# Kernel optimization log

Hardware: AMD Instinct MI355X
Metric: run time of the kernel (lower is better)

## Reference

```python
import jax, jax.numpy as jnp
import numpy as np

B, F, H, W = 2, 8, 16, 16
S = F * H * W                 # 2048 tokens
DIM, NH = 2048, 16
HD = DIM // NH                # 128
C = HD // 2                   # 64 complex pairs per head
CT = C - 2 * (C // 3)         # 22 temporal freqs
CH = C // 3                   # 21 height / 21 width freqs
L = 1024                      # freq table length
SHIFT = 4                     # TCROPE_SHIFT
EPS = 1e-6


def setup_inputs():
    key = jax.random.key(0)
    ks = jax.random.split(key, 12)
    lin = lambda k: jax.random.normal(k, (DIM, DIM), jnp.float32) / np.sqrt(DIM)
    x = jax.random.normal(ks[0], (B, S, DIM), jnp.float32)
    q_w, k_w, v_w, o_w = lin(ks[1]), lin(ks[2]), lin(ks[3]), lin(ks[4])
    q_b = jax.random.normal(ks[5], (DIM,), jnp.float32) * 0.02
    k_b = jax.random.normal(ks[6], (DIM,), jnp.float32) * 0.02
    v_b = jax.random.normal(ks[7], (DIM,), jnp.float32) * 0.02
    o_b = jax.random.normal(ks[8], (DIM,), jnp.float32) * 0.02
    norm_q_w = jnp.ones((DIM,), jnp.float32)
    norm_k_w = jnp.ones((DIM,), jnp.float32)
    # unit-magnitude complex rotations stored as (cos, sin): [L, C, 2]
    inv = 1.0 / (10000.0 ** (np.arange(C, dtype=np.float32) / C))
    ang = np.arange(L, dtype=np.float32)[:, None] * inv[None, :]
    freqs = jnp.asarray(np.stack([np.cos(ang), np.sin(ang)], axis=-1))
    seq_lens = jnp.full((B,), S, jnp.int32)
    grid_sizes = jnp.tile(jnp.array([[F, H, W]], jnp.int32), (B, 1))
    inner_t = jnp.array([[4, 4], [3, 5]], jnp.int32)  # per-sample shot lengths, sum == F
    return dict(x=x, q_w=q_w, q_b=q_b, k_w=k_w, k_b=k_b, v_w=v_w, v_b=v_b,
                o_w=o_w, o_b=o_b, norm_q_w=norm_q_w, norm_k_w=norm_k_w,
                freqs=freqs, seq_lens=seq_lens, grid_sizes=grid_sizes, inner_t=inner_t)


def _rmsnorm(x, w):
    return x * jax.lax.rsqrt(jnp.mean(x * x, axis=-1, keepdims=True) + EPS) * w


def _rope(x, freqs, inner_t, seq_lens):
    # x: [B,S,NH,HD]; per-sample 3D RoPE over (f,h,w) with per-shot temporal index shift.
    xr = x.reshape(B, S, NH, C, 2)
    f0, f1, f2 = freqs[:, :CT], freqs[:, CT:CT + CH], freqs[:, CT + CH:]
    t = jnp.arange(F)
    # frame t belongs to shot j  =>  temporal freq index = j*SHIFT + t  (matches freq_select)
    shot = jax.vmap(lambda it: jnp.searchsorted(jnp.cumsum(it), t, side='right'))(inner_t)
    t_idx = shot * SHIFT + t[None, :]                                   # [B,F]
    tf = jnp.broadcast_to(f0[t_idx][:, :, None, None], (B, F, H, W, CT, 2))
    hf = jnp.broadcast_to(f1[:H][None, None, :, None], (B, F, H, W, CH, 2))
    wf = jnp.broadcast_to(f2[:W][None, None, None, :], (B, F, H, W, CH, 2))
    fr = jnp.concatenate([tf, hf, wf], axis=-2).reshape(B, S, 1, C, 2)  # [B,S,1,C,2]
    a, b = xr[..., 0], xr[..., 1]
    cr, ci = fr[..., 0], fr[..., 1]
    rot = jnp.stack([a * cr - b * ci, a * ci + b * cr], axis=-1).reshape(B, S, NH, HD)
    # positions past f*h*w are left un-rotated in the original (tail concat)
    keep = (jnp.arange(S)[None, :] < seq_lens[:, None])[:, :, None, None]
    return jnp.where(keep, rot, x)


def reference(x, q_w, q_b, k_w, k_b, v_w, v_b, o_w, o_b,
              norm_q_w, norm_k_w, freqs, seq_lens, grid_sizes, inner_t):
    # grid_sizes is (F,H,W) for every sample; baked in as static constants above.
    q = _rmsnorm(x @ q_w + q_b, norm_q_w).reshape(B, S, NH, HD)
    k = _rmsnorm(x @ k_w + k_b, norm_k_w).reshape(B, S, NH, HD)
    v = (x @ v_w + v_b).reshape(B, S, NH, HD)
    q = _rope(q, freqs, inner_t, seq_lens)
    k = _rope(k, freqs, inner_t, seq_lens)
    scores = jnp.einsum('bqnd,bknd->bnqk', q, k) * (HD ** -0.5)
    kmask = (jnp.arange(S)[None, :] < seq_lens[:, None])[:, None, None, :]
    scores = jnp.where(kmask, scores, -1e30)
    attn = jax.nn.softmax(scores, axis=-1)
    out = jnp.einsum('bnqk,bknd->bqnd', attn, v).reshape(B, S, DIM)
    return out @ o_w + o_b
```

## Files before the change

### kernel.cpp

```cpp
#include <hip/hip_runtime.h>


typedef __attribute__((ext_vector_type(8))) short bf16x8;
typedef __attribute__((ext_vector_type(4))) float f32x4;

__device__ __forceinline__ unsigned short f2bf(float f) {
  unsigned int u = __builtin_bit_cast(unsigned int, f);
  u = (u + 0x7FFFu + ((u >> 16) & 1u)) >> 16;
  return (unsigned short)u;
}
__device__ __forceinline__ float bf2f(unsigned short h) {
  unsigned int u = ((unsigned int)h) << 16;
  return __builtin_bit_cast(float, u);
}

#define GLOAD16(gp, lp)                                                        \
  __builtin_amdgcn_global_load_lds(                                            \
      (__attribute__((address_space(1))) void*)(gp),                           \
      (__attribute__((address_space(3))) void*)(lp), 16, 0, 0)

__global__ __launch_bounds__(256) void k_convert(const float* __restrict__ in,
                                                 unsigned short* __restrict__ out,
                                                 int n8) {
  int i = blockIdx.x * 256 + threadIdx.x;
  const int stride = gridDim.x * 256;
  for (; i < n8; i += stride) {
    const float4* p = (const float4*)in + (size_t)i * 2;
    float4 a = p[0], b = p[1];
    bf16x8 v;
    v[0] = (short)f2bf(a.x); v[1] = (short)f2bf(a.y);
    v[2] = (short)f2bf(a.z); v[3] = (short)f2bf(a.w);
    v[4] = (short)f2bf(b.x); v[5] = (short)f2bf(b.y);
    v[6] = (short)f2bf(b.z); v[7] = (short)f2bf(b.w);
    *(bf16x8*)(out + (size_t)i * 8) = v;
  }
}

__global__ __launch_bounds__(256) void k_transpose(const float* __restrict__ in,
                                                   unsigned short* __restrict__ out,
                                                   int R, int C) {
  __shared__ float tile[32][33];
  const int c0 = blockIdx.x * 32, r0 = blockIdx.y * 32;
  const int tx = threadIdx.x, ty = threadIdx.y;
#pragma unroll
  for (int i = 0; i < 4; i++)
    tile[ty + i * 8][tx] = in[(size_t)(r0 + ty + i * 8) * C + c0 + tx];
  __syncthreads();
#pragma unroll
  for (int i = 0; i < 4; i++)
    out[(size_t)(c0 + ty + i * 8) * R + r0 + tx] = f2bf(tile[tx][ty + i * 8]);
}

template <int OUTF32, int BIASMODE>
__global__ __launch_bounds__(256) void k_gemm(const unsigned short* __restrict__ A,
                                              const unsigned short* __restrict__ BT,
                                              void* __restrict__ Cout,
                                              const float* __restrict__ bias,
                                              int M, int N, int K) {
  __shared__ unsigned short As[128 * 32];
  __shared__ unsigned short Bs[128 * 32];
  const int tid = threadIdx.x;
  const int lane = tid & 63, w = tid >> 6;
  const int g = lane >> 4, cc = lane & 15;
  const int gx = gridDim.x;
  int id = blockIdx.y * gx + blockIdx.x;
  const int tot = gx * gridDim.y;
  id = (id & 7) * (tot >> 3) + (id >> 3);
  const int n0 = (id % gx) * 128, m0 = (id / gx) * 128;
  const int wm = (w >> 1) * 64, wn = (w & 1) * 64;
  f32x4 acc[4][4] = {};
  const unsigned short* Ab = A + (size_t)m0 * K;
  const unsigned short* Bb = BT + (size_t)n0 * K;
  const int r0 = tid >> 2, c0 = (tid & 3) * 8;
  for (int kt = 0; kt < K; kt += 32) {
    GLOAD16(Ab + (size_t)r0 * K + kt + c0, As + tid * 8);
    GLOAD16(Ab + (size_t)(r0 + 64) * K + kt + c0, As + (tid + 256) * 8);
    GLOAD16(Bb + (size_t)r0 * K + kt + c0, Bs + tid * 8);
    GLOAD16(Bb + (size_t)(r0 + 64) * K + kt + c0, Bs + (tid + 256) * 8);
    __syncthreads();
    bf16x8 af[4], bfr[4];
#pragma unroll
    for (int m4 = 0; m4 < 4; m4++)
      af[m4] = *(const bf16x8*)(As + (wm + m4 * 16 + cc) * 32 + g * 8);
#pragma unroll
    for (int n4 = 0; n4 < 4; n4++)
      bfr[n4] = *(const bf16x8*)(Bs + (wn + n4 * 16 + cc) * 32 + g * 8);
#pragma unroll
    for (int m4 = 0; m4 < 4; m4++)
#pragma unroll
      for (int n4 = 0; n4 < 4; n4++)
        acc[m4][n4] = __builtin_amdgcn_mfma_f32_16x16x32_bf16(af[m4], bfr[n4],
                                                              acc[m4][n4], 0, 0, 0);
    __syncthreads();
  }
#pragma unroll
  for (int m4 = 0; m4 < 4; m4++)
#pragma unroll
    for (int n4 = 0; n4 < 4; n4++) {
      const int col = n0 + wn + n4 * 16 + cc;
#pragma unroll
      for (int r = 0; r < 4; r++) {
        const int row = m0 + wm + m4 * 16 + g * 4 + r;
        float v = acc[m4][n4][r];
        if (BIASMODE == 1) v += bias[row];
        if (BIASMODE == 2) v += bias[col];
        if (OUTF32)
          ((float*)Cout)[(size_t)row * N + col] = v;
        else
          ((unsigned short*)Cout)[(size_t)row * N + col] = f2bf(v);
      }
    }
}

__device__ __forceinline__ void stage_half(const unsigned short* __restrict__ src,
                                           int K, unsigned short* dst, int tid) {
#pragma unroll
  for (int j = 0; j < 2; j++) {
    const int li = tid + j * 512;
    const int r = li >> 3;
    const int c16 = (li & 7) ^ (r & 7);
    GLOAD16(src + (size_t)r * K + c16 * 8, (char*)dst + li * 16);
  }
}

__global__ __launch_bounds__(512, 2) void k_gemm_yqk(const unsigned short* __restrict__ A,
                                                     const unsigned short* __restrict__ BT,
                                                     unsigned short* __restrict__ Cout) {
  __shared__ unsigned short As[2][256 * 64];
  __shared__ unsigned short Bs[2][256 * 64];
  const int tid = threadIdx.x;
  const int lane = tid & 63, w = tid >> 6;
  const int g = lane >> 4, cc = lane & 15;
  const int wm = (w >> 2) * 128, wn = (w & 3) * 64;
  const int swz = (cc & 7) << 4;
  const int N = 4096, K = 2048;
  int id = blockIdx.x;
  id = (id & 7) * 32 + (id >> 3);
  const int m0 = (id >> 4) * 256, n0 = (id & 15) * 256;
  f32x4 acc[8][4] = {};
  const int T = K >> 6;

  stage_half(BT + (size_t)n0 * K, K, Bs[0], tid);
  stage_half(A + (size_t)m0 * K, K, As[0], tid);
  stage_half(BT + (size_t)(n0 + 128) * K, K, Bs[0] + 8192, tid);
  stage_half(A + (size_t)(m0 + 128) * K, K, As[0] + 8192, tid);
  stage_half(BT + (size_t)n0 * K + 64, K, Bs[1], tid);
  stage_half(A + (size_t)m0 * K + 64, K, As[1], tid);
  asm volatile("s_waitcnt vmcnt(4)" ::: "memory");
  __builtin_amdgcn_s_barrier();

  for (int t = 0; t < T; ++t) {
    const int c = t & 1;
    const char* Ac = (const char*)As[c];
    const char* Bc = (const char*)Bs[c];
    bf16x8 ar[4][2], br[4][2];
#pragma unroll
    for (int m = 0; m < 4; m++)
#pragma unroll
      for (int kk = 0; kk < 2; kk++)
        ar[m][kk] = *(const bf16x8*)(Ac + (wm + m * 16 + cc) * 128 +
                                     ((kk * 64 + g * 16) ^ swz));
#pragma unroll
    for (int n = 0; n < 2; n++)
#pragma unroll
      for (int kk = 0; kk < 2; kk++)
        br[n][kk] = *(const bf16x8*)(Bc + (wn + n * 16 + cc) * 128 +
                                     ((kk * 64 + g * 16) ^ swz));
    stage_half(BT + (size_t)(n0 + 128) * K + ((t + 1) & (T - 1)) * 64, K,
               Bs[c ^ 1] + 8192, tid);
    __builtin_amdgcn_s_barrier();
    asm volatile("s_waitcnt lgkmcnt(0)" ::: "memory");
    __builtin_amdgcn_sched_barrier(0);
    __builtin_amdgcn_s_setprio(1);
#pragma unroll
    for (int kk = 0; kk < 2; kk++)
#pragma unroll
      for (int m = 0; m < 4; m++)
#pragma unroll
        for (int n = 0; n < 2; n++)
          acc[m][n] = __builtin_amdgcn_mfma_f32_16x16x32_bf16(ar[m][kk], br[n][kk],
                                                              acc[m][n], 0, 0, 0);
    __builtin_amdgcn_s_setprio(0);
    __builtin_amdgcn_s_barrier();
#pragma unroll
    for (int n = 2; n < 4; n++)
#pragma unroll
      for (int kk = 0; kk < 2; kk++)
        br[n][kk] = *(const bf16x8*)(Bc + (wn + n * 16 + cc) * 128 +
                                     ((kk * 64 + g * 16) ^ swz));
    stage_half(A + (size_t)(m0 + 128) * K + ((t + 1) & (T - 1)) * 64, K,
               As[c ^ 1] + 8192, tid);
    __builtin_amdgcn_s_barrier();
    asm volatile("s_waitcnt lgkmcnt(0)" ::: "memory");
    __builtin_amdgcn_sched_barrier(0);
    __builtin_amdgcn_s_setprio(1);
#pragma unroll
    for (int kk = 0; kk < 2; kk++)
#pragma unroll
      for (int m = 0; m < 4; m++)
#pragma unroll
        for (int n = 2; n < 4; n++)
          acc[m][n] = __builtin_amdgcn_mfma_f32_16x16x32_bf16(ar[m][kk], br[n][kk],
                                                              acc[m][n], 0, 0, 0);
    __builtin_amdgcn_s_setprio(0);
    __builtin_amdgcn_s_barrier();
#pragma unroll
    for (int m = 0; m < 4; m++)
#pragma unroll
      for (int kk = 0; kk < 2; kk++)
        ar[m][kk] = *(const bf16x8*)(Ac + (wm + (m + 4) * 16 + cc) * 128 +
                                     ((kk * 64 + g * 16) ^ swz));
    stage_half(BT + (size_t)n0 * K + ((t + 2) & (T - 1)) * 64, K, Bs[c], tid);
    __builtin_amdgcn_s_barrier();
    asm volatile("s_waitcnt lgkmcnt(0)" ::: "memory");
    __builtin_amdgcn_sched_barrier(0);
    __builtin_amdgcn_s_setprio(1);
#pragma unroll
    for (int kk = 0; kk < 2; kk++)
#pragma unroll
      for (int m = 0; m < 4; m++)
#pragma unroll
        for (int n = 0; n < 2; n++)
          acc[m + 4][n] = __builtin_amdgcn_mfma_f32_16x16x32_bf16(ar[m][kk], br[n][kk],
                                                                  acc[m + 4][n], 0, 0, 0);
    __builtin_amdgcn_s_setprio(0);
    __builtin_amdgcn_s_barrier();
    stage_half(A + (size_t)m0 * K + ((t + 2) & (T - 1)) * 64, K, As[c], tid);
    __builtin_amdgcn_s_setprio(1);
#pragma unroll
    for (int kk = 0; kk < 2; kk++)
#pragma unroll
      for (int m = 0; m < 4; m++)
#pragma unroll
        for (int n = 2; n < 4; n++)
          acc[m + 4][n] = __builtin_amdgcn_mfma_f32_16x16x32_bf16(ar[m][kk], br[n][kk],
                                                                  acc[m + 4][n], 0, 0, 0);
    __builtin_amdgcn_s_setprio(0);
    if (t < T - 2)
      asm volatile("s_waitcnt vmcnt(4)" ::: "memory");
    else
      asm volatile("s_waitcnt vmcnt(0)" ::: "memory");
    __builtin_amdgcn_sched_barrier(0);
    __builtin_amdgcn_s_barrier();
  }

#pragma unroll
  for (int mi = 0; mi < 8; mi++)
#pragma unroll
    for (int n = 0; n < 4; n++) {
      const int col = n0 + wn + n * 16 + cc;
#pragma unroll
      for (int j = 0; j < 4; j++) {
        const int row = m0 + wm + mi * 16 + g * 4 + j;
        Cout[(size_t)row * N + col] = f2bf(acc[mi][n][j]);
      }
    }
}

__global__ __launch_bounds__(256) void k_qk_epi(const unsigned short* __restrict__ Yqk,
                                                const float* __restrict__ q_b,
                                                const float* __restrict__ k_b,
                                                const float* __restrict__ nqw,
                                                const float* __restrict__ nkw,
                                                const float* __restrict__ freqs,
                                                const int* __restrict__ inner_t,
                                                unsigned short* __restrict__ Q,
                                                unsigned short* __restrict__ K) {
  const int row = blockIdx.x;
  const int b = row >> 11, s = row & 2047;
  const int t = threadIdx.x;
  const unsigned short* yr = Yqk + (size_t)row * 4096;
  bf16x8 yq = *(const bf16x8*)(yr + t * 8);
  bf16x8 yk = *(const bf16x8*)(yr + 2048 + t * 8);
  float4 qb0 = *(const float4*)(q_b + t * 8), qb1 = *(const float4*)(q_b + t * 8 + 4);
  float4 kb0 = *(const float4*)(k_b + t * 8), kb1 = *(const float4*)(k_b + t * 8 + 4);
  float q[8], k[8];
  q[0] = bf2f((unsigned short)yq[0]) + qb0.x; q[1] = bf2f((unsigned short)yq[1]) + qb0.y;
  q[2] = bf2f((unsigned short)yq[2]) + qb0.z; q[3] = bf2f((unsigned short)yq[3]) + qb0.w;
  q[4] = bf2f((unsigned short)yq[4]) + qb1.x; q[5] = bf2f((unsigned short)yq[5]) + qb1.y;
  q[6] = bf2f((unsigned short)yq[6]) + qb1.z; q[7] = bf2f((unsigned short)yq[7]) + qb1.w;
  k[0] = bf2f((unsigned short)yk[0]) + kb0.x; k[1] = bf2f((unsigned short)yk[1]) + kb0.y;
  k[2] = bf2f((unsigned short)yk[2]) + kb0.z; k[3] = bf2f((unsigned short)yk[3]) + kb0.w;
  k[4] = bf2f((unsigned short)yk[4]) + kb1.x; k[5] = bf2f((unsigned short)yk[5]) + kb1.y;
  k[6] = bf2f((unsigned short)yk[6]) + kb1.z; k[7] = bf2f((unsigned short)yk[7]) + kb1.w;
  float ssq = 0.f, ssk = 0.f;
#pragma unroll
  for (int j = 0; j < 8; j++) { ssq += q[j] * q[j]; ssk += k[j] * k[j]; }
#pragma unroll
  for (int off = 32; off; off >>= 1) {
    ssq += __shfl_xor(ssq, off);
    ssk += __shfl_xor(ssk, off);
  }
  __shared__ float red[8];
  const int w = t >> 6;
  if ((t & 63) == 0) { red[w] = ssq; red[4 + w] = ssk; }
  __syncthreads();
  const float sq = red[0] + red[1] + red[2] + red[3];
  const float sk = red[4] + red[5] + red[6] + red[7];
  const float rq = __builtin_amdgcn_rsqf(sq * (1.0f / 2048.0f) + 1e-6f);
  const float rk = __builtin_amdgcn_rsqf(sk * (1.0f / 2048.0f) + 1e-6f);
  float4 nq0 = *(const float4*)(nqw + t * 8), nq1 = *(const float4*)(nqw + t * 8 + 4);
  float4 nk0 = *(const float4*)(nkw + t * 8), nk1 = *(const float4*)(nkw + t * 8 + 4);
  q[0] *= rq * nq0.x; q[1] *= rq * nq0.y; q[2] *= rq * nq0.z; q[3] *= rq * nq0.w;
  q[4] *= rq * nq1.x; q[5] *= rq * nq1.y; q[6] *= rq * nq1.z; q[7] *= rq * nq1.w;
  k[0] *= rk * nk0.x; k[1] *= rk * nk0.y; k[2] *= rk * nk0.z; k[3] *= rk * nk0.w;
  k[4] *= rk * nk1.x; k[5] *= rk * nk1.y; k[6] *= rk * nk1.z; k[7] *= rk * nk1.w;
  const int f = s >> 8, hh = (s >> 4) & 15, ww = s & 15;
  const int it0 = inner_t[b * 2], it1 = inner_t[b * 2 + 1];
  const int trow = ((f >= it0) + (f >= it0 + it1)) * 4 + f;
#pragma unroll
  for (int jj = 0; jj < 4; jj++) {
    const int c = (t * 4 + jj) & 63;
    const int fr = (c < 22) ? trow : ((c < 43) ? hh : ww);
    const float cr = freqs[((size_t)fr * 64 + c) * 2];
    const float ci = freqs[((size_t)fr * 64 + c) * 2 + 1];
    float a = q[2 * jj], bb = q[2 * jj + 1];
    q[2 * jj] = a * cr - bb * ci; q[2 * jj + 1] = a * ci + bb * cr;
    a = k[2 * jj]; bb = k[2 * jj + 1];
    k[2 * jj] = a * cr - bb * ci; k[2 * jj + 1] = a * ci + bb * cr;
  }
  const float QSCALE = 0.08838834764831845f * 1.4426950408889634f;
  bf16x8 oq, ok;
#pragma unroll
  for (int j = 0; j < 8; j++) {
    oq[j] = (short)f2bf(q[j] * QSCALE);
    ok[j] = (short)f2bf(k[j]);
  }
  const int head = t >> 4, d0 = (t & 15) * 8;
  const size_t off = ((size_t)(b * 16 + head) * 2048 + s) * 128 + d0;
  *(bf16x8*)(Q + off) = oq;
  *(bf16x8*)(K + off) = ok;
}

__global__ __launch_bounds__(512, 4) void k_attn(const unsigned short* __restrict__ Q,
                                                 const unsigned short* __restrict__ K,
                                                 const unsigned short* __restrict__ V,
                                                 unsigned short* __restrict__ O) {
  __shared__ unsigned short Ks[2][64 * 128];
  __shared__ unsigned short Vs[2][128 * 64];
  __shared__ unsigned short Ps[8 * 16 * 64];
  const int tid = threadIdx.x;
  const int lane = tid & 63, w = tid >> 6;
  const int g = lane >> 4, cc = lane & 15;
  const int q0 = blockIdx.x * 128;
  const int bh = blockIdx.y;
  const int b = bh >> 4, h = bh & 15;

  const unsigned short* Qb = Q + ((size_t)bh * 2048 + q0 + w * 16 + cc) * 128;
  bf16x8 qf[4];
#pragma unroll
  for (int kk = 0; kk < 4; kk++) qf[kk] = *(const bf16x8*)(Qb + kk * 32 + g * 8);

  const char* kbase = (const char*)(K + (size_t)bh * 2048 * 128);
  const char* vbase = (const char*)V + ((size_t)h * 128 * 4096 + (size_t)b * 2048) * 2;

  f32x4 acc[8] = {};
  float mloc = -3.0e38f, lloc = 0.f;
  char* Pb = (char*)Ps + w * 2048 + cc * 128;
  const int psw = (cc & 7) << 4;
  const int gbase = (lane & 48) | (((lane >> 4) & 3) << 2);
  const f32x4 vzero = {0.f, 0.f, 0.f, 0.f};

#define ATTN_STAGE(s0, bi)                                                     \
  {                                                                            \
    const char* kt0 = kbase + (size_t)(s0) * 256;                              \
    const char* vt0 = vbase + (size_t)(s0) * 2;                                \
    char* Kd = (char*)(Ks[bi]);                                                \
    char* Vd = (char*)(Vs[bi]);                                                \
    _Pragma("unroll") for (int i = 0; i < 2; i++) {                            \
      const int li = i * 512 + tid;                                            \
      const int kr = li >> 4;                                                  \
      const int kc = ((li & 15) * 16) ^ ((kr & 7) << 4);                       \
      GLOAD16(kt0 + kr * 256 + kc, Kd + li * 16);                              \
      const int vd = li >> 3;                                                  \
      const int vc = ((li & 7) * 16) ^ ((vd & 7) << 4);                        \
      GLOAD16(vt0 + (size_t)vd * 8192 + vc, Vd + li * 16);                     \
    }                                                                          \
  }

  ATTN_STAGE(0, 0);
  for (int t = 0; t < 32; ++t) {
    const int cur = t & 1;
    if (t < 31) {
      ATTN_STAGE((t + 1) * 64, cur ^ 1);
      asm volatile("s_waitcnt vmcnt(4)" ::: "memory");
    } else {
      asm volatile("s_waitcnt vmcnt(0)" ::: "memory");
    }
    __builtin_amdgcn_sched_barrier(0);
    __builtin_amdgcn_s_barrier();

    const char* kcur = (const char*)(Ks[cur]);
    const int sw = (cc & 7) << 4;
    f32x4 sf[4];
    __builtin_amdgcn_s_setprio(1);
#pragma unroll
    for (int n4 = 0; n4 < 4; n4++) {
      sf[n4] = vzero;
      const char* krow = kcur + (n4 * 16 + cc) * 256;
#pragma unroll
      for (int kk = 0; kk < 4; kk++) {
        bf16x8 kf = *(const bf16x8*)(krow + ((kk * 64 + g * 16) ^ sw));
        sf[n4] = __builtin_amdgcn_mfma_f32_16x16x32_bf16(kf, qf[kk], sf[n4], 0, 0, 0);
      }
    }
    __builtin_amdgcn_s_setprio(0);

    float tm = fmaxf(fmaxf(fmaxf(sf[0][0], sf[0][1]), fmaxf(sf[0][2], sf[0][3])),
                     fmaxf(fmaxf(sf[1][0], sf[1][1]), fmaxf(sf[1][2], sf[1][3])));
    tm = fmaxf(tm, fmaxf(fmaxf(fmaxf(sf[2][0], sf[2][1]), fmaxf(sf[2][2], sf[2][3])),
                         fmaxf(fmaxf(sf[3][0], sf[3][1]), fmaxf(sf[3][2], sf[3][3]))));
    tm = fmaxf(tm, __shfl_xor(tm, 16));
    tm = fmaxf(tm, __shfl_xor(tm, 32));
    if (__any(tm > mloc + 8.0f)) {
      const float mn = fmaxf(mloc, tm);
      const float sc = __builtin_amdgcn_exp2f(mloc - mn);
      mloc = mn;
      lloc *= sc;
      f32x4 scv;
#pragma unroll
      for (int r = 0; r < 4; r++) scv[r] = __shfl(sc, gbase + r);
#pragma unroll
      for (int d4 = 0; d4 < 8; d4++) acc[d4] *= scv;
    }
    float rs = 0.f;
#pragma unroll
    for (int n4 = 0; n4 < 4; n4++) {
      const float p0 = __builtin_amdgcn_exp2f(sf[n4][0] - mloc);
      const float p1 = __builtin_amdgcn_exp2f(sf[n4][1] - mloc);
      const float p2 = __builtin_amdgcn_exp2f(sf[n4][2] - mloc);
      const float p3 = __builtin_amdgcn_exp2f(sf[n4][3] - mloc);
      rs += (p0 + p1) + (p2 + p3);
      unsigned lo, hi;
      asm("v_cvt_pk_bf16_f32 %0, %1, %2" : "=v"(lo) : "v"(p0), "v"(p1));
      asm("v_cvt_pk_bf16_f32 %0, %1, %2" : "=v"(hi) : "v"(p2), "v"(p3));
      uint2 pv_; pv_.x = lo; pv_.y = hi;
      *(uint2*)(Pb + ((n4 * 32 + g * 8) ^ psw)) = pv_;
    }
    rs += __shfl_xor(rs, 16);
    rs += __shfl_xor(rs, 32);
    lloc += rs;

    const char* vcur = (const char*)(Vs[cur]);
    __builtin_amdgcn_s_setprio(1);
#pragma unroll
    for (int ks = 0; ks < 2; ks++) {
      bf16x8 pf = *(const bf16x8*)(Pb + ((ks * 64 + g * 16) ^ psw));
#pragma unroll
      for (int d4 = 0; d4 < 8; d4++) {
        const int dd = d4 * 16 + cc;
        bf16x8 vf = *(const bf16x8*)(vcur + dd * 128 +
                                     ((ks * 64 + g * 16) ^ ((dd & 7) << 4)));
        acc[d4] = __builtin_amdgcn_mfma_f32_16x16x32_bf16(pf, vf, acc[d4], 0, 0, 0);
      }
    }
    __builtin_amdgcn_s_setprio(0);

    asm volatile("s_waitcnt lgkmcnt(0)" ::: "memory");
    __builtin_amdgcn_sched_barrier(0);
    __builtin_amdgcn_s_barrier();
  }
#undef ATTN_STAGE

  const float invl = __builtin_amdgcn_rcpf(lloc);
  float ir[4];
#pragma unroll
  for (int r = 0; r < 4; r++) ir[r] = __shfl(invl, gbase + r);
  unsigned short* Ob = O + (size_t)(b * 2048 + q0 + w * 16) * 2048 + h * 128;
#pragma unroll
  for (int d4 = 0; d4 < 8; d4++)
#pragma unroll
    for (int r = 0; r < 4; r++)
      Ob[(size_t)(g * 4 + r) * 2048 + d4 * 16 + cc] = f2bf(acc[d4][r] * ir[r]);
}

extern "C" void kernel_launch(void* const* d_in, const int* in_sizes, int n_in,
                              void* d_out, int out_size, void* d_ws, size_t ws_size,
                              hipStream_t stream) {
  const float* x     = (const float*)d_in[0];
  const float* q_w   = (const float*)d_in[1];
  const float* q_b   = (const float*)d_in[2];
  const float* k_w   = (const float*)d_in[3];
  const float* k_b   = (const float*)d_in[4];
  const float* v_w   = (const float*)d_in[5];
  const float* v_b   = (const float*)d_in[6];
  const float* o_w   = (const float*)d_in[7];
  const float* o_b   = (const float*)d_in[8];
  const float* nqw   = (const float*)d_in[9];
  const float* nkw   = (const float*)d_in[10];
  const float* freqs = (const float*)d_in[11];
  const int* inner_t = (const int*)d_in[14];

  const size_t NEED = (size_t)112 << 20;
  if (ws_size < NEED) return;

  char* ws = (char*)d_ws;
  unsigned short* xb   = (unsigned short*)(ws);
  unsigned short* WqkT = (unsigned short*)(ws + ((size_t)16 << 20));
  unsigned short* WvT  = (unsigned short*)(ws + ((size_t)32 << 20));
  unsigned short* WoT  = (unsigned short*)(ws + ((size_t)40 << 20));
  unsigned short* Yqk  = (unsigned short*)(ws + ((size_t)48 << 20));
  unsigned short* Vt   = (unsigned short*)(ws + ((size_t)80 << 20));
  unsigned short* Kr   = (unsigned short*)(ws + ((size_t)96 << 20));
  unsigned short* Qr   = xb;
  unsigned short* Orow = WqkT;

  dim3 tb(32, 8);
  k_convert<<<2048, 256, 0, stream>>>(x, xb, 4096 * 2048 / 8);
  k_transpose<<<dim3(64, 64), tb, 0, stream>>>(q_w, WqkT, 2048, 2048);
  k_transpose<<<dim3(64, 64), tb, 0, stream>>>(k_w, WqkT + (size_t)2048 * 2048, 2048, 2048);
  k_transpose<<<dim3(64, 64), tb, 0, stream>>>(v_w, WvT, 2048, 2048);
  k_transpose<<<dim3(64, 64), tb, 0, stream>>>(o_w, WoT, 2048, 2048);
  k_gemm_yqk<<<256, 512, 0, stream>>>(xb, WqkT, Yqk);
  k_gemm<0, 1><<<dim3(32, 16), 256, 0, stream>>>(WvT, xb, Vt, v_b, 2048, 4096, 2048);
  k_qk_epi<<<4096, 256, 0, stream>>>(Yqk, q_b, k_b, nqw, nkw, freqs, inner_t, Qr, Kr);
  k_attn<<<dim3(16, 32), 512, 0, stream>>>(Qr, Kr, Vt, Orow);
  k_gemm<1, 2><<<dim3(16, 32), 256, 0, stream>>>(Orow, WoT, (float*)d_out, o_b, 4096, 2048, 2048);
}
```

Before: 320.2 us.

## Fuse weight transposes and input conversion into one prep kernel, remap attention blocks

Replaces the separate conversion kernel and four transpose launches with a single prep kernel that uses 64x64 tiles, float4 loads and 16-byte bf16 stores. The attention launch becomes one-dimensional with a block-index swizzle that spreads consecutive blocks across XCDs. The QK^T MFMA loop is reordered so all four K fragments are loaded per kk step, interleaving independent MFMAs. These aim to cut launch overhead, improve transpose memory efficiency and raise cache locality and ILP, at the cost of a larger shared tile and more register pressure.

```diff
diff --git a/kernel.cpp b/kernel.cpp
--- a/kernel.cpp
+++ b/kernel.cpp
@@ -19,36 +19,54 @@
       (__attribute__((address_space(1))) void*)(gp),                           \
       (__attribute__((address_space(3))) void*)(lp), 16, 0, 0)
 
-__global__ __launch_bounds__(256) void k_convert(const float* __restrict__ in,
-                                                 unsigned short* __restrict__ out,
-                                                 int n8) {
-  int i = blockIdx.x * 256 + threadIdx.x;
-  const int stride = gridDim.x * 256;
-  for (; i < n8; i += stride) {
-    const float4* p = (const float4*)in + (size_t)i * 2;
+__global__ __launch_bounds__(256) void k_prep(const float* __restrict__ x,
+                                              unsigned short* __restrict__ xb,
+                                              const float* __restrict__ qw,
+                                              const float* __restrict__ kw,
+                                              const float* __restrict__ vw,
+                                              const float* __restrict__ ow,
+                                              unsigned short* __restrict__ qkT,
+                                              unsigned short* __restrict__ vT,
+                                              unsigned short* __restrict__ oT) {
+  const int bid = blockIdx.x;
+  const int tid = threadIdx.x;
+  if (bid >= 4096) {
+    const int i = (bid - 4096) * 256 + tid;
+    const float4* p = (const float4*)x + (size_t)i * 2;
     float4 a = p[0], b = p[1];
     bf16x8 v;
     v[0] = (short)f2bf(a.x); v[1] = (short)f2bf(a.y);
     v[2] = (short)f2bf(a.z); v[3] = (short)f2bf(a.w);
     v[4] = (short)f2bf(b.x); v[5] = (short)f2bf(b.y);
     v[6] = (short)f2bf(b.z); v[7] = (short)f2bf(b.w);
-    *(bf16x8*)(out + (size_t)i * 8) = v;
-  }
-}
-
-__global__ __launch_bounds__(256) void k_transpose(const float* __restrict__ in,
-                                                   unsigned short* __restrict__ out,
-                                                   int R, int C) {
-  __shared__ float tile[32][33];
-  const int c0 = blockIdx.x * 32, r0 = blockIdx.y * 32;
-  const int tx = threadIdx.x, ty = threadIdx.y;
-#pragma unroll
-  for (int i = 0; i < 4; i++)
-    tile[ty + i * 8][tx] = in[(size_t)(r0 + ty + i * 8) * C + c0 + tx];
+    *(bf16x8*)(xb + (size_t)i * 8) = v;
+    return;
+  }
+  __shared__ float tile[64][65];
+  const int mat = bid >> 10, t10 = bid & 1023;
+  const float* in = (mat == 0) ? qw : (mat == 1) ? kw : (mat == 2) ? vw : ow;
+  unsigned short* out = (mat == 0) ? qkT
+                      : (mat == 1) ? (qkT + (size_t)2048 * 2048)
+                      : (mat == 2) ? vT : oT;
+  const int r0 = (t10 >> 5) * 64, c0 = (t10 & 31) * 64;
+#pragma unroll
+  for (int i = 0; i < 4; i++) {
+    const int fi = tid + i * 256;
+    const int row = fi >> 4, c4 = fi & 15;
+    float4 v = *(const float4*)(in + (size_t)(r0 + row) * 2048 + c0 + c4 * 4);
+    tile[row][c4 * 4 + 0] = v.x; tile[row][c4 * 4 + 1] = v.y;
+    tile[row][c4 * 4 + 2] = v.z; tile[row][c4 * 4 + 3] = v.w;
+  }
   __syncthreads();
 #pragma unroll
-  for (int i = 0; i < 4; i++)
-    out[(size_t)(c0 + ty + i * 8) * R + r0 + tx] = f2bf(tile[tx][ty + i * 8]);
+  for (int i = 0; i < 2; i++) {
+    const int oi = tid + i * 256;
+    const int c = oi >> 3, r8 = oi & 7;
+    bf16x8 o;
+#pragma unroll
+    for (int j = 0; j < 8; j++) o[j] = (short)f2bf(tile[r8 * 8 + j][c]);
+    *(bf16x8*)(out + (size_t)(c0 + c) * 2048 + r0 + r8 * 8) = o;
+  }
 }
 
 template <int OUTF32, int BIASMODE>
@@ -342,8 +360,10 @@
   const int tid = threadIdx.x;
   const int lane = tid & 63, w = tid >> 6;
   const int g = lane >> 4, cc = lane & 15;
-  const int q0 = blockIdx.x * 128;
-  const int bh = blockIdx.y;
+  const int orig = blockIdx.x;
+  const int lid = (orig & 7) * 64 + (orig >> 3);
+  const int bh = lid >> 4;
+  const int q0 = (lid & 15) * 128;
   const int b = bh >> 4, h = bh & 15;
 
   const unsigned short* Qb = Q + ((size_t)bh * 2048 + q0 + w * 16 + cc) * 128;
@@ -392,17 +412,19 @@
 
     const char* kcur = (const char*)(Ks[cur]);
     const int sw = (cc & 7) << 4;
-    f32x4 sf[4];
+    f32x4 sf[4] = {vzero, vzero, vzero, vzero};
     __builtin_amdgcn_s_setprio(1);
 #pragma unroll
-    for (int n4 = 0; n4 < 4; n4++) {
-      sf[n4] = vzero;
-      const char* krow = kcur + (n4 * 16 + cc) * 256;
-#pragma unroll
-      for (int kk = 0; kk < 4; kk++) {
-        bf16x8 kf = *(const bf16x8*)(krow + ((kk * 64 + g * 16) ^ sw));
-        sf[n4] = __builtin_amdgcn_mfma_f32_16x16x32_bf16(kf, qf[kk], sf[n4], 0, 0, 0);
-      }
+    for (int kk = 0; kk < 4; kk++) {
+      const int ko = (kk * 64 + g * 16) ^ sw;
+      bf16x8 kf0 = *(const bf16x8*)(kcur + (cc)*256 + ko);
+      bf16x8 kf1 = *(const bf16x8*)(kcur + (16 + cc) * 256 + ko);
+      bf16x8 kf2 = *(const bf16x8*)(kcur + (32 + cc) * 256 + ko);
+      bf16x8 kf3 = *(const bf16x8*)(kcur + (48 + cc) * 256 + ko);
+      sf[0] = __builtin_amdgcn_mfma_f32_16x16x32_bf16(kf0, qf[kk], sf[0], 0, 0, 0);
+      sf[1] = __builtin_amdgcn_mfma_f32_16x16x32_bf16(kf1, qf[kk], sf[1], 0, 0, 0);
+      sf[2] = __builtin_amdgcn_mfma_f32_16x16x32_bf16(kf2, qf[kk], sf[2], 0, 0, 0);
+      sf[3] = __builtin_amdgcn_mfma_f32_16x16x32_bf16(kf3, qf[kk], sf[3], 0, 0, 0);
     }
     __builtin_amdgcn_s_setprio(0);
 
@@ -505,15 +527,10 @@
   unsigned short* Qr   = xb;
   unsigned short* Orow = WqkT;
 
-  dim3 tb(32, 8);
-  k_convert<<<2048, 256, 0, stream>>>(x, xb, 4096 * 2048 / 8);
-  k_transpose<<<dim3(64, 64), tb, 0, stream>>>(q_w, WqkT, 2048, 2048);
-  k_transpose<<<dim3(64, 64), tb, 0, stream>>>(k_w, WqkT + (size_t)2048 * 2048, 2048, 2048);
-  k_transpose<<<dim3(64, 64), tb, 0, stream>>>(v_w, WvT, 2048, 2048);
-  k_transpose<<<dim3(64, 64), tb, 0, stream>>>(o_w, WoT, 2048, 2048);
+  k_prep<<<8192, 256, 0, stream>>>(x, xb, q_w, k_w, v_w, o_w, WqkT, WvT, WoT);
   k_gemm_yqk<<<256, 512, 0, stream>>>(xb, WqkT, Yqk);
   k_gemm<0, 1><<<dim3(32, 16), 256, 0, stream>>>(WvT, xb, Vt, v_b, 2048, 4096, 2048);
   k_qk_epi<<<4096, 256, 0, stream>>>(Yqk, q_b, k_b, nqw, nkw, freqs, inner_t, Qr, Kr);
-  k_attn<<<dim3(16, 32), 512, 0, stream>>>(Qr, Kr, Vt, Orow);
+  k_attn<<<512, 512, 0, stream>>>(Qr, Kr, Vt, Orow);
   k_gemm<1, 2><<<dim3(16, 32), 256, 0, stream>>>(Orow, WoT, (float*)d_out, o_b, 4096, 2048, 2048);
 }
```

New measurement: 313.6 us. 2.1% less time.
